# Performance work log

Measured on AMD Instinct MI355X. Metric: run time of the kernel, lower is better.

## Reference

```python
import jax, jax.numpy as jnp
import numpy as np

B, IN, H, L = 128, 256, 1024, 256
nA, nB = H // 2, (H - 1) // 2        # pairs per A-layer / B-layer
LB = L // 2
LA = L - LB                           # A layers come first when L is odd
PI = float(np.pi)


def setup_inputs() -> dict:
    key = jax.random.key(0)
    ks = jax.random.split(key, 14)
    u = lambda k, shp: jax.random.uniform(k, shp, minval=-PI, maxval=PI)
    return {
        "inputsR": jax.random.normal(ks[0], (B, IN), dtype=jnp.float32),
        "inputsI": jax.random.normal(ks[1], (B, IN), dtype=jnp.float32),
        "stateR": jax.random.normal(ks[2], (B, H), dtype=jnp.float32),
        "stateI": jax.random.normal(ks[3], (B, H), dtype=jnp.float32),
        # CLinear params (init_scale=0.01 inside RNNCellCmplx)
        "weightR": 0.01 * jax.random.normal(ks[4], (H, IN), dtype=jnp.float32),
        "weightI": 0.01 * jax.random.normal(ks[5], (H, IN), dtype=jnp.float32),
        "biasR": 0.01 * jax.random.normal(ks[6], (H,), dtype=jnp.float32),
        "biasI": 0.01 * jax.random.normal(ks[7], (H,), dtype=jnp.float32),
        # Clements mesh angles, uniform(-pi, pi)
        "angleA0": u(ks[8], (LA, nA)),
        "angleA1": u(ks[9], (LA, nA)),
        "angleB0": u(ks[10], (LB, nB)),
        "angleB1": u(ks[11], (LB, nB)),
        # diagonal phase + modReLU bias (both init to zero)
        "omega": jnp.zeros((H,), dtype=jnp.float32),
        "mod_bias": jnp.zeros((H,), dtype=jnp.float32),
    }


def _mzi(ar, ai, br, bi, th0, th1):
    """PSDC MZI on channel pairs: phase shifter e^{i*th0} on arm a, then a
    directional coupler with coupling angle th1 (unitary 2x2)."""
    c0, s0 = jnp.cos(th0), jnp.sin(th0)
    pr = c0 * ar - s0 * ai          # p = e^{i th0} * a
    pi_ = s0 * ar + c0 * ai
    c, s = jnp.cos(th1), jnp.sin(th1)
    oar = c * pr - s * bi           # a' = cos*p + i sin*b
    oai = c * pi_ + s * br
    obr = c * br - s * pi_          # b' = i sin*p + cos*b
    obi = c * bi + s * pr
    return oar, oai, obr, obi


def _layerA(xr, xi, t0, t1):
    Bs, N = xr.shape
    oar, oai, obr, obi = _mzi(xr[:, 0::2], xi[:, 0::2], xr[:, 1::2], xi[:, 1::2], t0, t1)
    xr = jnp.stack([oar, obr], axis=-1).reshape(Bs, N)
    xi = jnp.stack([oai, obi], axis=-1).reshape(Bs, N)
    return xr, xi


def _layerB(xr, xi, t0, t1):
    Bs, N = xr.shape  # pairs (1,2),(3,4),... ; channels 0 and N-1 pass through
    oar, oai, obr, obi = _mzi(xr[:, 1:-1:2], xi[:, 1:-1:2], xr[:, 2::2], xi[:, 2::2], t0, t1)
    midr = jnp.stack([oar, obr], axis=-1).reshape(Bs, N - 2)
    midi = jnp.stack([oai, obi], axis=-1).reshape(Bs, N - 2)
    xr = jnp.concatenate([xr[:, :1], midr, xr[:, -1:]], axis=1)
    xi = jnp.concatenate([xi[:, :1], midi, xi[:, -1:]], axis=1)
    return xr, xi


def _clements(xr, xi, A0, A1, B0, B1):
    def step(carry, ang):
        cr, ci = carry
        a0, a1, b0, b1 = ang
        cr, ci = _layerA(cr, ci, a0, a1)
        cr, ci = _layerB(cr, ci, b0, b1)
        return (cr, ci), None
    (xr, xi), _ = jax.lax.scan(step, (xr, xi), (A0[:LB], A1[:LB], B0, B1))
    for k in range(LB, LA):  # trailing A layer when num_layers is odd (static)
        xr, xi = _layerA(xr, xi, A0[k], A1[k])
    return xr, xi


def _forward(inputsR, inputsI, stateR, stateI, weightR, weightI, biasR, biasI,
             angleA0, angleA1, angleB0, angleB1, omega, mod_bias):
    # CLinear: complex y = W x + b
    ihR = inputsR @ weightR.T - inputsI @ weightI.T + biasR
    ihI = inputsR @ weightI.T + inputsI @ weightR.T + biasI
    # Clements unitary mesh on hidden state
    hr, hi = _clements(stateR, stateI, angleA0, angleA1, angleB0, angleB1)
    # diagonal phase e^{i omega}
    co, so = jnp.cos(omega), jnp.sin(omega)
    hhR = co * hr - so * hi
    hhI = so * hr + co * hi
    # complex add
    zr = ihR + hhR
    zi = ihI + hhI
    # modReLU: relu(|z| + b) * z / |z|
    mag = jnp.sqrt(zr * zr + zi * zi)
    scale = jax.nn.relu(mag + mod_bias) / jnp.maximum(mag, 1e-8)
    return jnp.stack([scale * zr, scale * zi])  # (2, B, H)


def reference(inputsR, inputsI, stateR, stateI, weightR, weightI, biasR, biasI,
              angleA0, angleA1, angleB0, angleB1, omega, mod_bias):
    return _forward(inputsR, inputsI, stateR, stateI, weightR, weightI, biasR, biasI,
                    angleA0, angleA1, angleB0, angleB1, omega, mod_bias)
```

## Files before the change

kernel.cpp:

```cpp
#include <hip/hip_runtime.h>
#include <math.h>

typedef float v2 __attribute__((ext_vector_type(2)));

#define NBATCH 128
#define NIN    256
#define NH     1024
#define NSTEPS 128
#define NB     511

#define TAB_F4_PER_L 1024
#define IH_OFF (NSTEPS * TAB_F4_PER_L * 4)

#define GEMM_BLOCKS 256
#define TRIG_BLOCKS 512

static __device__ __forceinline__ v2 to2(float a, float b) { v2 r; r.x = a; r.y = b; return r; }

__global__ __launch_bounds__(256) void prep_kernel(
    const float* __restrict__ inR, const float* __restrict__ inI,
    const float* __restrict__ wR,  const float* __restrict__ wI,
    const float* __restrict__ biasR, const float* __restrict__ biasI,
    const float* __restrict__ A0, const float* __restrict__ A1,
    const float* __restrict__ B0, const float* __restrict__ B1,
    float* __restrict__ ws)
{
    __shared__ v2 xs[256][17];
    __shared__ v2 wsh[32][34];

    if (blockIdx.x >= GEMM_BLOCKS) {
        int idx = (blockIdx.x - GEMM_BLOCKS) * 256 + threadIdx.x;
        int l = idx >> 10;
        int s = idx & 1023;
        int j = s >> 8, g = s & 255;
        float a0, a1;
        bool ident = false;
        if (j < 2) {
            int p = 2 * g + j;
            a0 = A0[l * 512 + p]; a1 = A1[l * 512 + p];
        } else {
            int p = 2 * g + (j - 2);
            if (p < NB) { a0 = B0[l * NB + p]; a1 = B1[l * NB + p]; }
            else ident = true;
        }
        float4 v;
        if (ident) v = make_float4(1.f, 0.f, 1.f, 0.f);
        else {
            float s0, c0, s1, c1;
            __sincosf(a0, &s0, &c0);
            __sincosf(a1, &s1, &c1);
            v = make_float4(c0, s0, c1, s1);
        }
        ((float4*)ws)[l * TAB_F4_PER_L + j * 256 + g] = v;
        return;
    }

    const int ht = blockIdx.x >> 3, bt = blockIdx.x & 7;
    const int h0 = ht * 32, b0 = bt * 16;
    const int tid = threadIdx.x;

    {
        int b = tid >> 4, k4 = tid & 15;
#pragma unroll
        for (int p = 0; p < 4; ++p) {
            int k0 = p * 64 + k4 * 4;
            float4 vr = *(const float4*)(inR + (b0 + b) * NIN + k0);
            float4 vi = *(const float4*)(inI + (b0 + b) * NIN + k0);
            xs[k0 + 0][b] = to2(vr.x, vi.x);
            xs[k0 + 1][b] = to2(vr.y, vi.y);
            xs[k0 + 2][b] = to2(vr.z, vi.z);
            xs[k0 + 3][b] = to2(vr.w, vi.w);
        }
    }

    const int hg = tid & 15, bl = tid >> 4;
    v2 acc0 = to2(0.f, 0.f), acc1 = to2(0.f, 0.f);

    for (int c = 0; c < 8; ++c) {
        __syncthreads();
        {
            int hh = tid >> 3, k4 = tid & 7;
            float4 vr = *(const float4*)(wR + (h0 + hh) * NIN + c * 32 + k4 * 4);
            float4 vi = *(const float4*)(wI + (h0 + hh) * NIN + c * 32 + k4 * 4);
            wsh[k4 * 4 + 0][hh] = to2(vr.x, vi.x);
            wsh[k4 * 4 + 1][hh] = to2(vr.y, vi.y);
            wsh[k4 * 4 + 2][hh] = to2(vr.z, vi.z);
            wsh[k4 * 4 + 3][hh] = to2(vr.w, vi.w);
        }
        __syncthreads();
#pragma unroll
        for (int k = 0; k < 32; ++k) {
            float4 wv = *(const float4*)&wsh[k][hg * 2];
            v2 w0 = to2(wv.x, wv.y), w1 = to2(wv.z, wv.w);
            v2 xv = xs[c * 32 + k][bl];
            acc0 += to2(xv.x, xv.x) * w0 + to2(xv.y, xv.y) * to2(-w0.y, w0.x);
            acc1 += to2(xv.x, xv.x) * w1 + to2(xv.y, xv.y) * to2(-w1.y, w1.x);
        }
    }
    int h = h0 + hg * 2, b = b0 + bl;
    acc0 += to2(biasR[h], biasI[h]);
    acc1 += to2(biasR[h + 1], biasI[h + 1]);
    ((float4*)(ws + IH_OFF))[b * 512 + (h >> 1)] =
        make_float4(acc0.x, acc0.y, acc1.x, acc1.y);
}

__device__ __forceinline__ void mzi(const float4 t, v2& a, v2& b)
{
    v2 P  = to2(t.x, t.y) * to2(a.x, a.x) + to2(-t.y, t.x) * to2(a.y, a.y);
    v2 na = to2(t.z, t.z) * P + to2(-t.w, t.w) * to2(b.y, b.x);
    b     = to2(t.z, t.z) * b + to2(-t.w, t.w) * to2(P.y, P.x);
    a = na;
}

__device__ __forceinline__ void stepf(v2 x[4], const float4* T, const float4 TL,
                                      int w, int lane, int par,
                                      v2 (*sx0)[3], v2 (*sx3)[3])
{
    mzi(T[0], x[0], x[1]);
    mzi(T[1], x[2], x[3]);
    if (lane == 0 && w > 0)  sx0[par][w - 1] = x[0];
    if (lane == 63 && w < 3) sx3[par][w] = x[3];
    __asm__ volatile("s_waitcnt lgkmcnt(0)" ::: "memory");
    __builtin_amdgcn_s_barrier();
    __asm__ volatile("" ::: "memory");

    float rcr = __shfl_down(x[0].x, 1, 64);
    float rci = __shfl_down(x[0].y, 1, 64);
    float lcr = __shfl_up(x[3].x, 1, 64);
    float lci = __shfl_up(x[3].y, 1, 64);
    if (lane == 63 && w < 3) { v2 t = sx0[par][w]; rcr = t.x; rci = t.y; }
    if (lane == 0 && w > 0)  { v2 t = sx3[par][w - 1]; lcr = t.x; lci = t.y; }

    mzi(T[2], x[1], x[2]);

    {
        const float4 t = T[3];
        v2 P = to2(t.x, t.y) * to2(x[3].x, x[3].x) + to2(-t.y, t.x) * to2(x[3].y, x[3].y);
        x[3] = to2(t.z, t.z) * P + to2(-t.w, t.w) * to2(rci, rcr);
    }
    {
        v2 P = to2(TL.x, TL.y) * to2(lcr, lcr) + to2(-TL.y, TL.x) * to2(lci, lci);
        x[0] = to2(TL.z, TL.z) * x[0] + to2(-TL.w, TL.w) * to2(P.y, P.x);
    }
}

#define LOADL(T, TL, l)                                                   \
    do {                                                                  \
        const float4* _p = tab + (l) * TAB_F4_PER_L + g;                  \
        T[0] = _p[0];                                                     \
        T[1] = _p[256];                                                   \
        T[2] = _p[512];                                                   \
        T[3] = _p[768];                                                   \
        TL = _p[767];                                     \
        if (g == 0) TL = make_float4(1.f, 0.f, 1.f, 0.f);                 \
    } while (0)

__global__ __launch_bounds__(256, 1) void mesh_kernel(
    const float* __restrict__ stateR, const float* __restrict__ stateI,
    const float* __restrict__ omega,  const float* __restrict__ mod_bias,
    const float* __restrict__ ws, float* __restrict__ out)
{
    const int b = blockIdx.x;
    const int g = threadIdx.x;
    const int lane = g & 63;
    const int w = g >> 6;
    const float4* tab = (const float4*)ws;

    __shared__ v2 sx0[2][3];
    __shared__ v2 sx3[2][3];

    v2 x[4];
    {
        float4 r = *(const float4*)(stateR + b * NH + 4 * g);
        float4 i = *(const float4*)(stateI + b * NH + 4 * g);
        x[0] = to2(r.x, i.x);
        x[1] = to2(r.y, i.y);
        x[2] = to2(r.z, i.z);
        x[3] = to2(r.w, i.w);
    }

    float4 Ta[4], Tb[4], TLa, TLb;
    LOADL(Ta, TLa, 0);
    for (int l = 0; l < NSTEPS; l += 2) {
        LOADL(Tb, TLb, l + 1);
        __builtin_amdgcn_sched_barrier(0);
        stepf(x, Ta, TLa, w, lane, 0, sx0, sx3);
        {
            int ln = (l + 2 < NSTEPS) ? l + 2 : NSTEPS - 1;
            LOADL(Ta, TLa, ln);
        }
        __builtin_amdgcn_sched_barrier(0);
        stepf(x, Tb, TLb, w, lane, 1, sx0, sx3);
    }

    float4 o4 = *(const float4*)(omega + 4 * g);
    float4 m4 = *(const float4*)(mod_bias + 4 * g);
    const float4* ihp = (const float4*)(ws + IH_OFF) + b * 512 + 2 * g;
    float4 ih0 = ihp[0], ih1 = ihp[1];

    float om[4] = { o4.x, o4.y, o4.z, o4.w };
    float mb[4] = { m4.x, m4.y, m4.z, m4.w };
    float ihr[4] = { ih0.x, ih0.z, ih1.x, ih1.z };
    float ihi[4] = { ih0.y, ih0.w, ih1.y, ih1.w };
    float oR[4], oI[4];
#pragma unroll
    for (int j = 0; j < 4; ++j) {
        float so, co;
        __sincosf(om[j], &so, &co);
        float zr = ihr[j] + co * x[j].x - so * x[j].y;
        float zi = ihi[j] + so * x[j].x + co * x[j].y;
        float mag = sqrtf(zr * zr + zi * zi);
        float sc = fmaxf(mag + mb[j], 0.f) / fmaxf(mag, 1e-8f);
        oR[j] = sc * zr;
        oI[j] = sc * zi;
    }
    *(float4*)(out + b * NH + 4 * g) = make_float4(oR[0], oR[1], oR[2], oR[3]);
    *(float4*)(out + NBATCH * NH + b * NH + 4 * g) = make_float4(oI[0], oI[1], oI[2], oI[3]);
}

extern "C" void kernel_launch(void* const* d_in, const int* in_sizes, int n_in,
                              void* d_out, int out_size, void* d_ws, size_t ws_size,
                              hipStream_t stream)
{
    const float* inputsR = (const float*)d_in[0];
    const float* inputsI = (const float*)d_in[1];
    const float* stateR  = (const float*)d_in[2];
    const float* stateI  = (const float*)d_in[3];
    const float* weightR = (const float*)d_in[4];
    const float* weightI = (const float*)d_in[5];
    const float* biasR   = (const float*)d_in[6];
    const float* biasI   = (const float*)d_in[7];
    const float* angleA0 = (const float*)d_in[8];
    const float* angleA1 = (const float*)d_in[9];
    const float* angleB0 = (const float*)d_in[10];
    const float* angleB1 = (const float*)d_in[11];
    const float* omega   = (const float*)d_in[12];
    const float* mod_b   = (const float*)d_in[13];
    float* ws = (float*)d_ws;
    float* out = (float*)d_out;

    hipLaunchKernelGGL(prep_kernel, dim3(GEMM_BLOCKS + TRIG_BLOCKS), dim3(256),
                       0, stream, inputsR, inputsI, weightR, weightI,
                       biasR, biasI, angleA0, angleA1, angleB0, angleB1, ws);
    hipLaunchKernelGGL(mesh_kernel, dim3(NBATCH), dim3(256), 0, stream,
                       stateR, stateI, omega, mod_b, ws, out);
}
```

Measured before the change: 151.3 us.

## Process two batch rows per mesh block to share angle loads and barriers

Each mesh_kernel block now carries two batch rows through the Clements mesh, so every trig-table load and every block barrier per layer is shared by both rows, and the grid is halved to 64 blocks. This roughly halves table traffic per row and the number of barrier waits relative to useful arithmetic, and gives more independent instructions to hide latency. The trade-off is half as many blocks on a chip with many CUs and a serial chain per block that is now twice as long in ALU work, plus more register pressure.

Measured after the change: 159.9 us. +5.7%, slower.

```diff
diff --git a/kernel.cpp b/kernel.cpp
--- a/kernel.cpp
+++ b/kernel.cpp
@@ -112,35 +112,49 @@
     a = na;
 }
 
-__device__ __forceinline__ void stepf(v2 x[4], const float4* T, const float4 TL,
+__device__ __forceinline__ void step2(v2 x0[4], v2 x1[4],
+                                      const float4* T, const float4 TL,
                                       int w, int lane, int par,
-                                      v2 (*sx0)[3], v2 (*sx3)[3])
-{
-    mzi(T[0], x[0], x[1]);
-    mzi(T[1], x[2], x[3]);
-    if (lane == 0 && w > 0)  sx0[par][w - 1] = x[0];
-    if (lane == 63 && w < 3) sx3[par][w] = x[3];
+                                      v2 (*sx0)[2][3], v2 (*sx3)[2][3])
+{
+    mzi(T[0], x0[0], x0[1]);
+    mzi(T[1], x0[2], x0[3]);
+    mzi(T[0], x1[0], x1[1]);
+    mzi(T[1], x1[2], x1[3]);
+    if (lane == 0 && w > 0)  { sx0[0][par][w - 1] = x0[0]; sx0[1][par][w - 1] = x1[0]; }
+    if (lane == 63 && w < 3) { sx3[0][par][w] = x0[3];     sx3[1][par][w] = x1[3]; }
     __asm__ volatile("s_waitcnt lgkmcnt(0)" ::: "memory");
     __builtin_amdgcn_s_barrier();
     __asm__ volatile("" ::: "memory");
 
-    float rcr = __shfl_down(x[0].x, 1, 64);
-    float rci = __shfl_down(x[0].y, 1, 64);
-    float lcr = __shfl_up(x[3].x, 1, 64);
-    float lci = __shfl_up(x[3].y, 1, 64);
-    if (lane == 63 && w < 3) { v2 t = sx0[par][w]; rcr = t.x; rci = t.y; }
-    if (lane == 0 && w > 0)  { v2 t = sx3[par][w - 1]; lcr = t.x; lci = t.y; }
-
-    mzi(T[2], x[1], x[2]);
+    float rcr0 = __shfl_down(x0[0].x, 1, 64), rci0 = __shfl_down(x0[0].y, 1, 64);
+    float lcr0 = __shfl_up(x0[3].x, 1, 64),   lci0 = __shfl_up(x0[3].y, 1, 64);
+    float rcr1 = __shfl_down(x1[0].x, 1, 64), rci1 = __shfl_down(x1[0].y, 1, 64);
+    float lcr1 = __shfl_up(x1[3].x, 1, 64),   lci1 = __shfl_up(x1[3].y, 1, 64);
+    if (lane == 63 && w < 3) {
+        v2 t0 = sx0[0][par][w]; rcr0 = t0.x; rci0 = t0.y;
+        v2 t1 = sx0[1][par][w]; rcr1 = t1.x; rci1 = t1.y;
+    }
+    if (lane == 0 && w > 0) {
+        v2 t0 = sx3[0][par][w - 1]; lcr0 = t0.x; lci0 = t0.y;
+        v2 t1 = sx3[1][par][w - 1]; lcr1 = t1.x; lci1 = t1.y;
+    }
+
+    mzi(T[2], x0[1], x0[2]);
+    mzi(T[2], x1[1], x1[2]);
 
     {
         const float4 t = T[3];
-        v2 P = to2(t.x, t.y) * to2(x[3].x, x[3].x) + to2(-t.y, t.x) * to2(x[3].y, x[3].y);
-        x[3] = to2(t.z, t.z) * P + to2(-t.w, t.w) * to2(rci, rcr);
+        v2 P0 = to2(t.x, t.y) * to2(x0[3].x, x0[3].x) + to2(-t.y, t.x) * to2(x0[3].y, x0[3].y);
+        x0[3] = to2(t.z, t.z) * P0 + to2(-t.w, t.w) * to2(rci0, rcr0);
+        v2 P1 = to2(t.x, t.y) * to2(x1[3].x, x1[3].x) + to2(-t.y, t.x) * to2(x1[3].y, x1[3].y);
+        x1[3] = to2(t.z, t.z) * P1 + to2(-t.w, t.w) * to2(rci1, rcr1);
     }
     {
-        v2 P = to2(TL.x, TL.y) * to2(lcr, lcr) + to2(-TL.y, TL.x) * to2(lci, lci);
-        x[0] = to2(TL.z, TL.z) * x[0] + to2(-TL.w, TL.w) * to2(P.y, P.x);
+        v2 P0 = to2(TL.x, TL.y) * to2(lcr0, lcr0) + to2(-TL.y, TL.x) * to2(lci0, lci0);
+        x0[0] = to2(TL.z, TL.z) * x0[0] + to2(-TL.w, TL.w) * to2(P0.y, P0.x);
+        v2 P1 = to2(TL.x, TL.y) * to2(lcr1, lcr1) + to2(-TL.y, TL.x) * to2(lci1, lci1);
+        x1[0] = to2(TL.z, TL.z) * x1[0] + to2(-TL.w, TL.w) * to2(P1.y, P1.x);
     }
 }
 
@@ -155,67 +169,79 @@
         if (g == 0) TL = make_float4(1.f, 0.f, 1.f, 0.f);                 \
     } while (0)
 
+__device__ __forceinline__ void loadx(v2 X[4], const float* __restrict__ stateR,
+                                      const float* __restrict__ stateI,
+                                      int row, int g)
+{
+    float4 r = *(const float4*)(stateR + row * NH + 4 * g);
+    float4 i = *(const float4*)(stateI + row * NH + 4 * g);
+    X[0] = to2(r.x, i.x);
+    X[1] = to2(r.y, i.y);
+    X[2] = to2(r.z, i.z);
+    X[3] = to2(r.w, i.w);
+}
+
 __global__ __launch_bounds__(256, 1) void mesh_kernel(
     const float* __restrict__ stateR, const float* __restrict__ stateI,
     const float* __restrict__ omega,  const float* __restrict__ mod_bias,
     const float* __restrict__ ws, float* __restrict__ out)
 {
-    const int b = blockIdx.x;
+    const int r0 = 2 * blockIdx.x, r1 = r0 + 1;
     const int g = threadIdx.x;
     const int lane = g & 63;
     const int w = g >> 6;
     const float4* tab = (const float4*)ws;
 
-    __shared__ v2 sx0[2][3];
-    __shared__ v2 sx3[2][3];
-
-    v2 x[4];
-    {
-        float4 r = *(const float4*)(stateR + b * NH + 4 * g);
-        float4 i = *(const float4*)(stateI + b * NH + 4 * g);
-        x[0] = to2(r.x, i.x);
-        x[1] = to2(r.y, i.y);
-        x[2] = to2(r.z, i.z);
-        x[3] = to2(r.w, i.w);
-    }
+    __shared__ v2 sx0[2][2][3];
+    __shared__ v2 sx3[2][2][3];
+
+    v2 x0[4], x1[4];
+    loadx(x0, stateR, stateI, r0, g);
+    loadx(x1, stateR, stateI, r1, g);
 
     float4 Ta[4], Tb[4], TLa, TLb;
     LOADL(Ta, TLa, 0);
     for (int l = 0; l < NSTEPS; l += 2) {
         LOADL(Tb, TLb, l + 1);
         __builtin_amdgcn_sched_barrier(0);
-        stepf(x, Ta, TLa, w, lane, 0, sx0, sx3);
+        step2(x0, x1, Ta, TLa, w, lane, 0, sx0, sx3);
         {
             int ln = (l + 2 < NSTEPS) ? l + 2 : NSTEPS - 1;
             LOADL(Ta, TLa, ln);
         }
         __builtin_amdgcn_sched_barrier(0);
-        stepf(x, Tb, TLb, w, lane, 1, sx0, sx3);
+        step2(x0, x1, Tb, TLb, w, lane, 1, sx0, sx3);
     }
 
     float4 o4 = *(const float4*)(omega + 4 * g);
     float4 m4 = *(const float4*)(mod_bias + 4 * g);
-    const float4* ihp = (const float4*)(ws + IH_OFF) + b * 512 + 2 * g;
-    float4 ih0 = ihp[0], ih1 = ihp[1];
-
     float om[4] = { o4.x, o4.y, o4.z, o4.w };
     float mb[4] = { m4.x, m4.y, m4.z, m4.w };
-    float ihr[4] = { ih0.x, ih0.z, ih1.x, ih1.z };
-    float ihi[4] = { ih0.y, ih0.w, ih1.y, ih1.w };
-    float oR[4], oI[4];
-#pragma unroll
-    for (int j = 0; j < 4; ++j) {
-        float so, co;
-        __sincosf(om[j], &so, &co);
-        float zr = ihr[j] + co * x[j].x - so * x[j].y;
-        float zi = ihi[j] + so * x[j].x + co * x[j].y;
-        float mag = sqrtf(zr * zr + zi * zi);
-        float sc = fmaxf(mag + mb[j], 0.f) / fmaxf(mag, 1e-8f);
-        oR[j] = sc * zr;
-        oI[j] = sc * zi;
-    }
-    *(float4*)(out + b * NH + 4 * g) = make_float4(oR[0], oR[1], oR[2], oR[3]);
-    *(float4*)(out + NBATCH * NH + b * NH + 4 * g) = make_float4(oI[0], oI[1], oI[2], oI[3]);
+    float so[4], co[4];
+#pragma unroll
+    for (int j = 0; j < 4; ++j) __sincosf(om[j], &so[j], &co[j]);
+
+#pragma unroll
+    for (int r = 0; r < 2; ++r) {
+        const int row = r0 + r;
+        const v2* xx = (r == 0) ? x0 : x1;
+        const float4* ihp = (const float4*)(ws + IH_OFF) + row * 512 + 2 * g;
+        float4 ih0 = ihp[0], ih1 = ihp[1];
+        float ihr[4] = { ih0.x, ih0.z, ih1.x, ih1.z };
+        float ihi[4] = { ih0.y, ih0.w, ih1.y, ih1.w };
+        float oR[4], oI[4];
+#pragma unroll
+        for (int j = 0; j < 4; ++j) {
+            float zr = ihr[j] + co[j] * xx[j].x - so[j] * xx[j].y;
+            float zi = ihi[j] + so[j] * xx[j].x + co[j] * xx[j].y;
+            float mag = sqrtf(zr * zr + zi * zi);
+            float sc = fmaxf(mag + mb[j], 0.f) / fmaxf(mag, 1e-8f);
+            oR[j] = sc * zr;
+            oI[j] = sc * zi;
+        }
+        *(float4*)(out + row * NH + 4 * g) = make_float4(oR[0], oR[1], oR[2], oR[3]);
+        *(float4*)(out + NBATCH * NH + row * NH + 4 * g) = make_float4(oI[0], oI[1], oI[2], oI[3]);
+    }
 }
 
 extern "C" void kernel_launch(void* const* d_in, const int* in_sizes, int n_in,
@@ -242,6 +268,6 @@
     hipLaunchKernelGGL(prep_kernel, dim3(GEMM_BLOCKS + TRIG_BLOCKS), dim3(256),
                        0, stream, inputsR, inputsI, weightR, weightI,
                        biasR, biasI, angleA0, angleA1, angleB0, angleB1, ws);
-    hipLaunchKernelGGL(mesh_kernel, dim3(NBATCH), dim3(256), 0, stream,
+    hipLaunchKernelGGL(mesh_kernel, dim3(NBATCH / 2), dim3(256), 0, stream,
                        stateR, stateI, omega, mod_b, ws, out);
 }
```
